# Performance work log

Hardware: AMD Instinct MI355X
Metric: run time of the kernel (lower is better)

## Reference

```python
import jax, jax.numpy as jnp
import numpy as np

THRESHOLD = 1.0  # CIF firing threshold (init kwarg)


def setup_inputs() -> dict:
    key = jax.random.key(0)
    k1, k2 = jax.random.split(key)
    B, T, H = 32, 2048, 512
    return {
        "hidden": jax.random.normal(k1, (B, T, H), dtype=jnp.float32),
        "alphas": jax.random.uniform(k2, (B, T), dtype=jnp.float32),
        "integrate": jnp.zeros((B,), dtype=jnp.float32),
        "frame": jnp.zeros((B, H), dtype=jnp.float32),
    }


def cif_scan(hidden, alphas, integrate, frame, threshold):
    """Continuous integrate-and-fire recurrence over time, vectorized over batch.

    hidden: [B,T,H], alphas: [B,T], integrate: [B], frame: [B,H]
    Returns fires [B,T], frames [B,T,H], integrate_new [B], frame_new [B,H].
    """

    def step(carry, inp):
        integ, fr = carry          # [B], [B,H]
        alpha, h_t = inp           # [B], [B,H]
        dist_completion = 1.0 - integ
        integ = integ + alpha
        fire = integ >= threshold                       # [B] bool
        integ_next = jnp.where(fire, integ - 1.0, integ)
        cur = jnp.where(fire, dist_completion, alpha)   # weight spent this step
        rem = alpha - cur                               # leftover weight after firing
        fr_out = fr + cur[:, None] * h_t                # frame recorded at this step
        fr_next = jnp.where(fire[:, None], rem[:, None] * h_t, fr_out)
        return (integ_next, fr_next), (integ, fr_out)

    xs = (jnp.swapaxes(alphas, 0, 1), jnp.swapaxes(hidden, 0, 1))  # time-major
    (integ_f, frame_f), (fires_t, frames_t) = jax.lax.scan(step, (integrate, frame), xs)
    fires = jnp.swapaxes(fires_t, 0, 1)    # [B,T]
    frames = jnp.swapaxes(frames_t, 0, 1)  # [B,T,H]
    return fires, frames, integ_f, frame_f


def reference(hidden, alphas, integrate, frame):
    T = hidden.shape[1]
    fires, frames, integ_new, frame_new = cif_scan(hidden, alphas, integrate, frame, THRESHOLD)
    # torch.index_select(frames[0], 0, nonzero(fires[0] >= threshold)) -> data-dependent
    # shape; emulate with jit-safe padded nonzero (padding rows replicate row 0).
    idx = jnp.nonzero(fires[0] >= THRESHOLD, size=T, fill_value=0)[0]
    frame_sel = frames[0][idx]  # [T, H], first num_fires rows are the fired frames
    return frame_sel, integ_new, frame_new
```

## Files before the change

### kernel.cpp

```cpp
#include <hip/hip_runtime.h>


#define THRESH 1.0f
#define MAXB   64
#define MAXT   2048
#define MAXCH  (MAXT / 64)

__device__ __forceinline__ float fract_exact(float x) {
    float r; asm("v_fract_f32 %0, %1" : "=v"(r) : "v"(x)); return r;
}

__global__ __launch_bounds__(512, 2) void cif_prep_kernel(
    const float4* __restrict__ a4,
    const float*  __restrict__ integ0,
    float4* __restrict__ aT4,
    float*  __restrict__ gT,
    int* __restrict__ rowStart, int* __restrict__ rowEnd, int* __restrict__ rowFlags,
    int* __restrict__ tlast,
    float* __restrict__ integ_out,
    int B, int T)
{
    const int tid = threadIdx.x;
    const int T4 = T >> 2;
    const int nchunk = T >> 6;

    __shared__ float              s_ci[MAXCH * MAXB];
    __shared__ unsigned long long s_mask[MAXCH * MAXB];
    __shared__ int                s_fire[MAXT];
    __shared__ int                s_nf, s_f0;

    for (int i = tid; i < B * T4; i += 512) {
        const int b = i / T4, c = i - b * T4;
        aT4[(size_t)c * B + b] = a4[i];
    }
    __syncthreads();

    if (tid < 64) {
        const int lane = tid;
        const bool act = lane < B;
        float integ = act ? integ0[lane] : 0.0f;
        float4 bufA[16], bufB[16];

#define LOADCH(buf, c) do { if (act) { \
        _Pragma("unroll") for (int j = 0; j < 16; ++j) \
            buf[j] = aT4[(size_t)((c) * 16 + j) * B + lane]; } } while (0)

#define DOCH(buf, c) do { if (act) { \
        s_ci[(c) * B + lane] = integ; \
        _Pragma("unroll") for (int j = 0; j < 16; ++j) { \
            integ = fract_exact(integ + buf[j].x); \
            integ = fract_exact(integ + buf[j].y); \
            integ = fract_exact(integ + buf[j].z); \
            integ = fract_exact(integ + buf[j].w); \
        } } } while (0)

        LOADCH(bufA, 0);
        for (int c = 0; c < nchunk; c += 2) {
            if (c + 1 < nchunk) LOADCH(bufB, c + 1);
            DOCH(bufA, c);
            if (c + 2 < nchunk) LOADCH(bufA, c + 2);
            if (c + 1 < nchunk) DOCH(bufB, c + 1);
        }
#undef LOADCH
#undef DOCH
        if (act) integ_out[lane] = integ;
    }
    __syncthreads();

    for (int w = tid; w < nchunk * B; w += 512) {
        const int c = w / B, b = w - c * B;
        float integ = s_ci[w];
        unsigned long long m = 0;
        for (int j = 0; j < 16; ++j) {
            const float4 av4 = aT4[(size_t)(c * 16 + j) * B + b];
            const float av[4] = {av4.x, av4.y, av4.z, av4.w};
            float gv[4];
#pragma unroll
            for (int k = 0; k < 4; ++k) {
                const int idx = j * 4 + k;
                const float alpha = av[k];
                const float s   = integ + alpha;
                const bool fire = (s >= THRESH);
                const float sm1 = s - 1.0f;
                integ = fire ? sm1 : s;
                gv[k] = fire ? sm1 : alpha;
                m |= fire ? (1ull << idx) : 0ull;
            }
#pragma unroll
            for (int k = 0; k < 4; ++k)
                gT[(size_t)(c * 64 + j * 4 + k) * B + b] = gv[k];
        }
        s_mask[w] = m;
    }
    __syncthreads();

    if (tid < B) {
        int tl = -1;
        for (int c = nchunk - 1; c >= 0; --c) {
            const unsigned long long mc = s_mask[c * B + tid];
            if (mc) { tl = c * 64 + 63 - __clzll(mc); break; }
        }
        tlast[tid] = tl;
    }
    if (tid < 64) {
        unsigned long long m0 = (tid < nchunk) ? s_mask[tid * B] : 0ull;
        const int pc = __popcll(m0);
        int x = pc;
#pragma unroll
        for (int d = 1; d < 64; d <<= 1) {
            const int y = __shfl_up(x, d);
            if (tid >= d) x += y;
        }
        if (tid == 63) s_nf = x;
        if (tid == 0)  s_f0 = (int)(m0 & 1ull);
        int r = x - pc;
        while (m0) {
            const int p = __ffsll(m0) - 1;
            s_fire[r++] = tid * 64 + p;
            m0 &= m0 - 1;
        }
    }
    __syncthreads();

    const int nf = s_nf, f0 = s_f0;
    for (int r = tid; r < T; r += 512) {
        int st, en, fl;
        if (r < nf) {
            en = s_fire[r];
            st = (r == 0) ? 0 : s_fire[r - 1];
            fl = ((r == 0) ? 1 : 0) | 2;
        } else {
            st = 0; en = 0; fl = 1 | (f0 ? 2 : 0);
        }
        rowStart[r] = st; rowEnd[r] = en; rowFlags[r] = fl;
    }
}

__global__ __launch_bounds__(128) void cif_out_kernel(
    const float* __restrict__ hidden,
    const float* __restrict__ frame0,
    const float* __restrict__ gT,
    const float* __restrict__ alphas,
    const int* __restrict__ rowStart, const int* __restrict__ rowEnd,
    const int* __restrict__ rowFlags, const int* __restrict__ tlast,
    float* __restrict__ out_sel,
    float* __restrict__ frame_out,
    int B, int T, int H)
{
    const int blk = blockIdx.x;

    if (blk < T) {
        const int r = blk;
        const int start = rowStart[r], end = rowEnd[r], fl = rowFlags[r];
        const float a  = alphas[end];
        const float ge = gT[(size_t)end * B];
        const float wend = (fl & 2) ? (a - ge) : a;
        for (int h0 = threadIdx.x * 4; h0 < H; h0 += 128 * 4) {
            float4 acc = (fl & 1) ? *reinterpret_cast<const float4*>(frame0 + h0)
                                  : make_float4(0.f, 0.f, 0.f, 0.f);
            for (int s = start; s < end; ++s) {
                const float  w  = gT[(size_t)s * B];
                const float4 hv = *reinterpret_cast<const float4*>(hidden + (size_t)s * H + h0);
                acc.x += w * hv.x; acc.y += w * hv.y;
                acc.z += w * hv.z; acc.w += w * hv.w;
            }
            const float4 hv = *reinterpret_cast<const float4*>(hidden + (size_t)end * H + h0);
            acc.x += wend * hv.x; acc.y += wend * hv.y;
            acc.z += wend * hv.z; acc.w += wend * hv.w;
            *reinterpret_cast<float4*>(out_sel + (size_t)r * H + h0) = acc;
        }
    } else {
        const int b  = blk - T;
        const int tl = tlast[b];
        const int start = (tl < 0) ? 0 : tl;
        const float* hb = hidden + (size_t)b * T * H;
        for (int h0 = threadIdx.x * 4; h0 < H; h0 += 128 * 4) {
            float4 acc = (tl < 0) ? *reinterpret_cast<const float4*>(frame0 + (size_t)b * H + h0)
                                  : make_float4(0.f, 0.f, 0.f, 0.f);
            for (int s = start; s < T; ++s) {
                const float  w  = gT[(size_t)s * B + b];
                const float4 hv = *reinterpret_cast<const float4*>(hb + (size_t)s * H + h0);
                acc.x += w * hv.x; acc.y += w * hv.y;
                acc.z += w * hv.z; acc.w += w * hv.w;
            }
            *reinterpret_cast<float4*>(frame_out + (size_t)b * H + h0) = acc;
        }
    }
}

extern "C" void kernel_launch(void* const* d_in, const int* in_sizes, int n_in,
                              void* d_out, int out_size, void* d_ws, size_t ws_size,
                              hipStream_t stream) {
    const float* hidden    = (const float*)d_in[0];
    const float* alphas    = (const float*)d_in[1];
    const float* integrate = (const float*)d_in[2];
    const float* frame     = (const float*)d_in[3];

    const int B = in_sizes[2];
    const int T = in_sizes[1] / B;
    const int H = in_sizes[3] / B;

    float* out       = (float*)d_out;
    float* out_sel   = out;
    float* integ_out = out + (size_t)T * H;
    float* frame_out = integ_out + B;

    char* ws = (char*)d_ws;
    float4* aT4   = (float4*)ws;  ws += sizeof(float) * (size_t)B * T;
    float*  gT    = (float*)ws;   ws += sizeof(float) * (size_t)B * T;
    int* rowStart = (int*)ws;     ws += sizeof(int) * T;
    int* rowEnd   = (int*)ws;     ws += sizeof(int) * T;
    int* rowFlags = (int*)ws;     ws += sizeof(int) * T;
    int* tlast    = (int*)ws;     ws += sizeof(int) * B;

    cif_prep_kernel<<<1, 512, 0, stream>>>(
        (const float4*)alphas, integrate, aT4, gT,
        rowStart, rowEnd, rowFlags, tlast, integ_out, B, T);

    cif_out_kernel<<<T + B, 128, 0, stream>>>(
        hidden, frame, gT, alphas, rowStart, rowEnd, rowFlags, tlast,
        out_sel, frame_out, B, T, H);
}
```

Baseline: 242.6 us.

## Stage alphas through double-buffered LDS with producer warps feeding the serial scan

The serial integrate scan in the prep kernel used to read transposed alphas directly from global memory with register double-buffering. Now the other wavefronts (tid>=64) copy the next super-chunk of alphas into one of two shared-memory buffers while the first wavefront scans the current buffer from LDS. This is meant to hide global-load latency on the single-wave critical path, at the cost of 64 KB of LDS and a block-wide barrier per super-chunk.

New measurement: 227.7 us. 1.07x faster.

```diff
diff --git a/kernel.cpp b/kernel.cpp
--- a/kernel.cpp
+++ b/kernel.cpp
@@ -5,6 +5,7 @@
 #define MAXB   64
 #define MAXT   2048
 #define MAXCH  (MAXT / 64)
+#define SC4    2048
 
 __device__ __forceinline__ float fract_exact(float x) {
     float r; asm("v_fract_f32 %0, %1" : "=v"(r) : "v"(x)); return r;
@@ -24,6 +25,8 @@
     const int T4 = T >> 2;
     const int nchunk = T >> 6;
 
+    __shared__ float4             s_abuf0[SC4];
+    __shared__ float4             s_abuf1[SC4];
     __shared__ float              s_ci[MAXCH * MAXB];
     __shared__ unsigned long long s_mask[MAXCH * MAXB];
     __shared__ int                s_fire[MAXT];
@@ -35,41 +38,48 @@
     }
     __syncthreads();
 
-    if (tid < 64) {
-        const int lane = tid;
-        const bool act = lane < B;
-        float integ = act ? integ0[lane] : 0.0f;
-        float4 bufA[16], bufB[16];
-
-#define LOADCH(buf, c) do { if (act) { \
-        _Pragma("unroll") for (int j = 0; j < 16; ++j) \
-            buf[j] = aT4[(size_t)((c) * 16 + j) * B + lane]; } } while (0)
-
-#define DOCH(buf, c) do { if (act) { \
-        s_ci[(c) * B + lane] = integ; \
-        _Pragma("unroll") for (int j = 0; j < 16; ++j) { \
-            integ = fract_exact(integ + buf[j].x); \
-            integ = fract_exact(integ + buf[j].y); \
-            integ = fract_exact(integ + buf[j].z); \
-            integ = fract_exact(integ + buf[j].w); \
-        } } } while (0)
-
-        LOADCH(bufA, 0);
-        for (int c = 0; c < nchunk; c += 2) {
-            if (c + 1 < nchunk) LOADCH(bufB, c + 1);
-            DOCH(bufA, c);
-            if (c + 2 < nchunk) LOADCH(bufA, c + 2);
-            if (c + 1 < nchunk) DOCH(bufB, c + 1);
-        }
-#undef LOADCH
-#undef DOCH
-        if (act) integ_out[lane] = integ;
-    }
-    __syncthreads();
+    const int SPS = (SC4 * 4) / B;
+    const int NSC = T / SPS;
+    const int cpsc = SPS >> 6;
+
+    for (int i = tid; i < SC4; i += 512) s_abuf0[i] = aT4[i];
+    __syncthreads();
+
+    float integ = (tid < B) ? integ0[tid] : 0.0f;
+
+    for (int sc = 0; sc < NSC; ++sc) {
+        if (tid >= 64) {
+            if (sc + 1 < NSC) {
+                const float4* src = aT4 + (size_t)(sc + 1) * SC4;
+                float4* dst = (sc & 1) ? s_abuf0 : s_abuf1;
+                for (int i = tid - 64; i < SC4; i += 448) dst[i] = src[i];
+            }
+        } else if (tid < B) {
+            const float4* sb = (sc & 1) ? s_abuf1 : s_abuf0;
+            const int cbase = sc * cpsc;
+            for (int cl = 0; cl < cpsc; ++cl) {
+                s_ci[(cbase + cl) * B + tid] = integ;
+                float4 rb[16];
+#pragma unroll
+                for (int j = 0; j < 16; ++j)
+                    rb[j] = sb[(cl * 16 + j) * B + tid];
+                __builtin_amdgcn_sched_barrier(0);
+#pragma unroll
+                for (int j = 0; j < 16; ++j) {
+                    integ = fract_exact(integ + rb[j].x);
+                    integ = fract_exact(integ + rb[j].y);
+                    integ = fract_exact(integ + rb[j].z);
+                    integ = fract_exact(integ + rb[j].w);
+                }
+            }
+        }
+        __syncthreads();
+    }
+    if (tid < B) integ_out[tid] = integ;
 
     for (int w = tid; w < nchunk * B; w += 512) {
         const int c = w / B, b = w - c * B;
-        float integ = s_ci[w];
+        float ig = s_ci[w];
         unsigned long long m = 0;
         for (int j = 0; j < 16; ++j) {
             const float4 av4 = aT4[(size_t)(c * 16 + j) * B + b];
@@ -79,10 +89,10 @@
             for (int k = 0; k < 4; ++k) {
                 const int idx = j * 4 + k;
                 const float alpha = av[k];
-                const float s   = integ + alpha;
+                const float s   = ig + alpha;
                 const bool fire = (s >= THRESH);
                 const float sm1 = s - 1.0f;
-                integ = fire ? sm1 : s;
+                ig = fire ? sm1 : s;
                 gv[k] = fire ? sm1 : alpha;
                 m |= fire ? (1ull << idx) : 0ull;
             }
```
